# Performance work log

Hardware: AMD Instinct MI355X
Metric: run time of the kernel (lower is better)

## Reference

```python
import jax, jax.numpy as jnp
import numpy as np


def _pairwise_smooth_l1_sum(x):
    # x: [N, D]. All N^2 ordered pairs (i, j), including i == j (diff = 0),
    # matching torch's full index_select over [i for i ... for j ...].
    d = x[:, None, :] - x[None, :, :]            # [N, N, D]
    ad = jnp.abs(d)
    # SmoothL1 with beta = 1 (torch default): 0.5*d^2 if |d| < 1 else |d| - 0.5
    sl1 = jnp.where(ad < 1.0, 0.5 * d * d, ad - 0.5)
    return jnp.sum(sl1, axis=-1).reshape(-1)     # [N*N]


def setup_inputs() -> dict:
    key = jax.random.key(0)
    k1, k2 = jax.random.split(key)
    N, D = 512, 512
    teacher = jax.random.normal(k1, (N, D), dtype=jnp.float32)
    student = jax.random.normal(k2, (N, D), dtype=jnp.float32)
    return {"teacher": teacher, "student": student}


def reference(teacher, student):
    teacher_l2s = _pairwise_smooth_l1_sum(teacher)
    teacher_l2s = teacher_l2s / jnp.mean(teacher_l2s)
    student_l2s = _pairwise_smooth_l1_sum(student)
    student_l2s = student_l2s / jnp.mean(student_l2s)
    return jnp.sum(jnp.abs(teacher_l2s - student_l2s))
```

## Files before the change

### kernel.cpp

```cpp
#include <hip/hip_runtime.h>

#define N 512
#define D 512
#define TILE 32
#define DC 64
#define PITCH 68
#define NT 16
#define NTILES 136
#define NSLICE 8

__device__ __forceinline__ void sl1(float& acc, float x, float y) {
    float d  = x - y;
    float ad = fabsf(d);
    float m  = fminf(ad, 1.0f);
    acc = fmaf(m, fmaf(2.0f, ad, -m), acc);
}

__global__ __launch_bounds__(256, 8) void pair_sums_kernel(
    const float* __restrict__ Tm, const float* __restrict__ Sm,
    float* __restrict__ P, float* __restrict__ sums)
{
    const int mat = blockIdx.z;
    const float* __restrict__ X = mat ? Sm : Tm;
    float* __restrict__ Pm = P + (size_t)mat * (N * N);

    int rem = blockIdx.x, ti = 0;
    while (rem >= NT - ti) { rem -= NT - ti; ++ti; }
    const int tj = ti + rem;
    const int i0 = ti * TILE, j0 = tj * TILE;
    const int d0 = blockIdx.y * DC;

    __shared__ float Xi[TILE][PITCH];
    __shared__ float Xj[TILE][PITCH];

    const int t  = threadIdx.x;
    const int tx = t & 15;
    const int ty = t >> 4;

    #pragma unroll
    for (int kk = 0; kk < 2; ++kk) {
        int idx = t + kk * 256;
        int row = idx >> 4;
        int c4  = (idx & 15) * 4;
        *(float4*)&Xi[row][c4] = *(const float4*)&X[(size_t)(i0 + row) * D + d0 + c4];
        *(float4*)&Xj[row][c4] = *(const float4*)&X[(size_t)(j0 + row) * D + d0 + c4];
    }
    __syncthreads();

    float a00 = 0.f, a01 = 0.f, a10 = 0.f, a11 = 0.f;
    #pragma unroll 4
    for (int d4 = 0; d4 < DC / 4; ++d4) {
        float4 p0 = *(const float4*)&Xi[ty][d4 * 4];
        float4 p1 = *(const float4*)&Xi[ty + 16][d4 * 4];
        float4 q0 = *(const float4*)&Xj[tx][d4 * 4];
        float4 q1 = *(const float4*)&Xj[tx + 16][d4 * 4];
        sl1(a00, p0.x, q0.x); sl1(a00, p0.y, q0.y); sl1(a00, p0.z, q0.z); sl1(a00, p0.w, q0.w);
        sl1(a01, p0.x, q1.x); sl1(a01, p0.y, q1.y); sl1(a01, p0.z, q1.z); sl1(a01, p0.w, q1.w);
        sl1(a10, p1.x, q0.x); sl1(a10, p1.y, q0.y); sl1(a10, p1.z, q0.z); sl1(a10, p1.w, q0.w);
        sl1(a11, p1.x, q1.x); sl1(a11, p1.y, q1.y); sl1(a11, p1.z, q1.z); sl1(a11, p1.w, q1.w);
    }

    const bool diag = (ti == tj);
    const bool w00 = !diag || (ty <= tx);
    const bool w10 = !diag;
    const float s00 = 0.5f * a00, s01 = 0.5f * a01, s10 = 0.5f * a10, s11 = 0.5f * a11;

    float bs = 0.f;
    if (w00) { atomicAdd(&Pm[(i0 + ty     ) * N + (j0 + tx     )], s00); bs += s00; }
              { atomicAdd(&Pm[(i0 + ty     ) * N + (j0 + tx + 16)], s01); bs += s01; }
    if (w10) { atomicAdd(&Pm[(i0 + ty + 16) * N + (j0 + tx     )], s10); bs += s10; }
    if (w00) { atomicAdd(&Pm[(i0 + ty + 16) * N + (j0 + tx + 16)], s11); bs += s11; }

    #pragma unroll
    for (int off = 32; off > 0; off >>= 1) bs += __shfl_down(bs, off, 64);
    __shared__ float wpart[4];
    if ((t & 63) == 0) wpart[t >> 6] = bs;
    __syncthreads();
    if (t == 0) atomicAdd(&sums[mat], wpart[0] + wpart[1] + wpart[2] + wpart[3]);
}

__global__ __launch_bounds__(256) void final_kernel(
    const float* __restrict__ P, const float* __restrict__ sums, float* __restrict__ out)
{
    const float NN = (float)N * (float)N;
    const float cT = NN / (2.0f * sums[0]);
    const float cS = NN / (2.0f * sums[1]);
    float local = 0.0f;
    const int nvec = N * N / 4;
    for (int v = blockIdx.x * 256 + threadIdx.x; v < nvec; v += gridDim.x * 256) {
        int i  = v >> 7;
        int jb = (v & 127) * 4;
        if (jb + 3 < i) continue;
        float4 tq = ((const float4*)P)[v];
        float4 sq = ((const float4*)(P + (size_t)N * N))[v];
        if (jb + 0 >= i) local += fabsf(tq.x * cT - sq.x * cS);
        if (jb + 1 >= i) local += fabsf(tq.y * cT - sq.y * cS);
        if (jb + 2 >= i) local += fabsf(tq.z * cT - sq.z * cS);
        if (jb + 3 >= i) local += fabsf(tq.w * cT - sq.w * cS);
    }
    #pragma unroll
    for (int off = 32; off > 0; off >>= 1) local += __shfl_down(local, off, 64);
    __shared__ float wpart[4];
    if ((threadIdx.x & 63) == 0) wpart[threadIdx.x >> 6] = local;
    __syncthreads();
    if (threadIdx.x == 0) atomicAdd(out, 2.0f * (wpart[0] + wpart[1] + wpart[2] + wpart[3]));
}

extern "C" void kernel_launch(void* const* d_in, const int* in_sizes, int n_in,
                              void* d_out, int out_size, void* d_ws, size_t ws_size,
                              hipStream_t stream) {
    const float* teacher = (const float*)d_in[0];
    const float* student = (const float*)d_in[1];
    float* out  = (float*)d_out;
    float* P    = (float*)d_ws;
    float* sums = P + 2 * (size_t)N * N;

    hipMemsetAsync(d_ws, 0, (2 * (size_t)N * N + 2) * sizeof(float), stream);
    hipMemsetAsync(d_out, 0, sizeof(float), stream);

    dim3 grid(NTILES, NSLICE, 2);
    pair_sums_kernel<<<grid, 256, 0, stream>>>(teacher, student, P, sums);
    final_kernel<<<128, 256, 0, stream>>>(P, sums, out);
}
```

Baseline: 97.52 us.

## Replace atomic accumulation with per-slice partial buffers reduced in final kernel

```diff
diff --git a/kernel.cpp b/kernel.cpp
--- a/kernel.cpp
+++ b/kernel.cpp
@@ -16,19 +16,21 @@
     acc = fmaf(m, fmaf(2.0f, ad, -m), acc);
 }
 
+
 __global__ __launch_bounds__(256, 8) void pair_sums_kernel(
     const float* __restrict__ Tm, const float* __restrict__ Sm,
-    float* __restrict__ P, float* __restrict__ sums)
+    float* __restrict__ Pp, float* __restrict__ sums)
 {
     const int mat = blockIdx.z;
+    const int sl  = blockIdx.y;
     const float* __restrict__ X = mat ? Sm : Tm;
-    float* __restrict__ Pm = P + (size_t)mat * (N * N);
+    float* __restrict__ Pm = Pp + (size_t)(mat * NSLICE + sl) * (N * N);
 
     int rem = blockIdx.x, ti = 0;
     while (rem >= NT - ti) { rem -= NT - ti; ++ti; }
     const int tj = ti + rem;
     const int i0 = ti * TILE, j0 = tj * TILE;
-    const int d0 = blockIdx.y * DC;
+    const int d0 = sl * DC;
 
     __shared__ float Xi[TILE][PITCH];
     __shared__ float Xj[TILE][PITCH];
@@ -66,10 +68,10 @@
     const float s00 = 0.5f * a00, s01 = 0.5f * a01, s10 = 0.5f * a10, s11 = 0.5f * a11;
 
     float bs = 0.f;
-    if (w00) { atomicAdd(&Pm[(i0 + ty     ) * N + (j0 + tx     )], s00); bs += s00; }
-              { atomicAdd(&Pm[(i0 + ty     ) * N + (j0 + tx + 16)], s01); bs += s01; }
-    if (w10) { atomicAdd(&Pm[(i0 + ty + 16) * N + (j0 + tx     )], s10); bs += s10; }
-    if (w00) { atomicAdd(&Pm[(i0 + ty + 16) * N + (j0 + tx + 16)], s11); bs += s11; }
+    if (w00) { Pm[(i0 + ty     ) * N + (j0 + tx     )] = s00; bs += s00; }
+              { Pm[(i0 + ty     ) * N + (j0 + tx + 16)] = s01; bs += s01; }
+    if (w10) { Pm[(i0 + ty + 16) * N + (j0 + tx     )] = s10; bs += s10; }
+    if (w00) { Pm[(i0 + ty + 16) * N + (j0 + tx + 16)] = s11; bs += s11; }
 
     #pragma unroll
     for (int off = 32; off > 0; off >>= 1) bs += __shfl_down(bs, off, 64);
@@ -80,7 +82,7 @@
 }
 
 __global__ __launch_bounds__(256) void final_kernel(
-    const float* __restrict__ P, const float* __restrict__ sums, float* __restrict__ out)
+    const float* __restrict__ Pp, const float* __restrict__ sums, float* __restrict__ out)
 {
     const float NN = (float)N * (float)N;
     const float cT = NN / (2.0f * sums[0]);
@@ -91,8 +93,15 @@
         int i  = v >> 7;
         int jb = (v & 127) * 4;
         if (jb + 3 < i) continue;
-        float4 tq = ((const float4*)P)[v];
-        float4 sq = ((const float4*)(P + (size_t)N * N))[v];
+        float4 tq = make_float4(0.f, 0.f, 0.f, 0.f);
+        float4 sq = make_float4(0.f, 0.f, 0.f, 0.f);
+        #pragma unroll
+        for (int s = 0; s < NSLICE; ++s) {
+            float4 a = ((const float4*)(Pp + (size_t)s * (N * N)))[v];
+            float4 b = ((const float4*)(Pp + (size_t)(NSLICE + s) * (N * N)))[v];
+            tq.x += a.x; tq.y += a.y; tq.z += a.z; tq.w += a.w;
+            sq.x += b.x; sq.y += b.y; sq.z += b.z; sq.w += b.w;
+        }
         if (jb + 0 >= i) local += fabsf(tq.x * cT - sq.x * cS);
         if (jb + 1 >= i) local += fabsf(tq.y * cT - sq.y * cS);
         if (jb + 2 >= i) local += fabsf(tq.z * cT - sq.z * cS);
@@ -112,13 +121,13 @@
     const float* teacher = (const float*)d_in[0];
     const float* student = (const float*)d_in[1];
     float* out  = (float*)d_out;
-    float* P    = (float*)d_ws;
-    float* sums = P + 2 * (size_t)N * N;
+    float* Pp   = (float*)d_ws;
+    float* sums = Pp + (size_t)2 * NSLICE * N * N;
 
-    hipMemsetAsync(d_ws, 0, (2 * (size_t)N * N + 2) * sizeof(float), stream);
+    hipMemsetAsync(sums, 0, 2 * sizeof(float), stream);
     hipMemsetAsync(d_out, 0, sizeof(float), stream);
 
     dim3 grid(NTILES, NSLICE, 2);
-    pair_sums_kernel<<<grid, 256, 0, stream>>>(teacher, student, P, sums);
-    final_kernel<<<128, 256, 0, stream>>>(P, sums, out);
+    pair_sums_kernel<<<grid, 256, 0, stream>>>(teacher, student, Pp, sums);
+    final_kernel<<<256, 256, 0, stream>>>(Pp, sums, out);
 }
```

New measurement: 97.87 us. About the same (+0.4%).
